# Performance work log

Measured on AMD Instinct MI355X. Metric: run time of the kernel, lower is better.

The kernel has to match this reference:

```python
import jax, jax.numpy as jnp
import numpy as np

N, M, D = 2048, 100000, 128
K = 5


def setup_inputs() -> dict:
    key = jax.random.key(0)
    k1, k2 = jax.random.split(key)
    features = jax.random.normal(k1, (N, D), dtype=jnp.float32)
    memory_bank = jax.random.normal(k2, (M, D), dtype=jnp.float32)
    # normalization buffers computed during fit(); use plausible scalars
    min_val = jnp.zeros((), dtype=jnp.float32)
    max_val = jnp.ones((), dtype=jnp.float32)
    return {
        "features": features,
        "memory_bank": memory_bank,
        "min_val": min_val,
        "max_val": max_val,
        "n_neighbors": K,
    }


def reference(features, memory_bank, min_val, max_val, n_neighbors):
    x2 = jnp.sum(features * features, axis=1, keepdims=True)        # (N,1)
    y2 = jnp.sum(memory_bank * memory_bank, axis=1)[None, :]        # (1,M)
    d2 = x2 + y2 - 2.0 * (features @ memory_bank.T)                 # (N,M)
    dist = jnp.sqrt(jnp.maximum(d2, 0.0))
    # k smallest distances per query (topk largest=False)
    neg_knn, _ = jax.lax.top_k(-dist, n_neighbors)                  # (N,K)
    knn = -neg_knn
    # min-max normalization with fitted stats
    knn = (knn - min_val) / (max_val - min_val)
    return knn.mean(axis=1)                                         # (N,)
```

## Files before the change

### kernel.cpp

```cpp
#include <hip/hip_runtime.h>
#include <stdint.h>

#define N_Q 2048
#define M_B 100000
#define D_DIM 128
#define KNN 5
#define SLABS_TOTAL 1563
#define M_PAD (SLABS_TOTAL * 64)
#define CHUNKS 56
#define SPC 28
#define PPC 14
#define FTOT (CHUNKS * PPC)
#define ROWBLOCKS 16
#define TROWS 128
#define BIGF 3.0e38f
#define NEGF -3.0e38f


typedef __attribute__((ext_vector_type(8))) short short8;
typedef __attribute__((ext_vector_type(4))) unsigned short ushort4v;
typedef __attribute__((ext_vector_type(8))) unsigned short ushort8v;
typedef __attribute__((ext_vector_type(4))) float f32x4;

static __device__ __forceinline__ unsigned short f2bf(float f) {
  unsigned int u = __builtin_bit_cast(unsigned int, f);
  u = (u + 0x7FFFu + ((u >> 16) & 1u)) >> 16;
  return (unsigned short)u;
}

static __device__ __forceinline__ void gload_lds16(const void* g, void* l) {
  __builtin_amdgcn_global_load_lds((const __attribute__((address_space(1))) unsigned int*)g,
                                   (__attribute__((address_space(3))) unsigned int*)l, 16, 0, 0);
}
static __device__ __forceinline__ void gload_lds4(const void* g, void* l) {
  __builtin_amdgcn_global_load_lds((const __attribute__((address_space(1))) unsigned int*)g,
                                   (__attribute__((address_space(3))) unsigned int*)l, 4, 0, 0);
}

#define DPPMAX(v, ctrl)                                                              \
  do {                                                                               \
    int _t = __builtin_amdgcn_update_dpp(0, __builtin_bit_cast(int, (v)), (ctrl),    \
                                         0xf, 0xf, false);                           \
    (v) = fmaxf((v), __builtin_bit_cast(float, _t));                                 \
  } while (0)
#define DPPADD(v, ctrl)                                                              \
  do {                                                                               \
    int _t = __builtin_amdgcn_update_dpp(0, __builtin_bit_cast(int, (v)), (ctrl),    \
                                         0xf, 0xf, false);                           \
    (v) = (v) + __builtin_bit_cast(float, _t);                                       \
  } while (0)

__global__ __launch_bounds__(256) void k_prep(const float* __restrict__ Y,
                                              unsigned short* __restrict__ ybf,
                                              float* __restrict__ ny2) {
  const int s = blockIdx.x;
  const int t = threadIdx.x;
  __shared__ __align__(16) unsigned short tile[8192];
  __shared__ float redy[64 * 33];
#pragma unroll
  for (int i = 0; i < 8; ++i) {
    const int u = i * 256 + t;
    const int rowl = u >> 5;
    const int q = u & 31;
    const int rowg = s * 64 + rowl;
    const int rowc = (rowg < M_B) ? rowg : (M_B - 1);
    const float4 v = ((const float4*)Y)[(size_t)rowc * 32 + q];
    redy[rowl * 33 + q] = v.x * v.x + v.y * v.y + v.z * v.z + v.w * v.w;
    ushort4v o;
    o[0] = f2bf(v.x); o[1] = f2bf(v.y); o[2] = f2bf(v.z); o[3] = f2bf(v.w);
    *(ushort4v*)(tile + (size_t)(((q >> 1) * 64 + rowl) * 8 + (q & 1) * 4)) = o;
  }
  __syncthreads();
  {
    const int rowl = t >> 2;
    const int k = t & 3;
    float ss = 0.f;
#pragma unroll
    for (int j = 0; j < 8; ++j) ss += redy[rowl * 33 + k * 8 + j];
    DPPADD(ss, 0xB1);
    DPPADD(ss, 0x4E);
    const int rowg = s * 64 + rowl;
    if ((t & 3) == 0) ny2[(size_t)s * 64 + rowl] = (rowg < M_B) ? (-0.5f * ss) : NEGF;
  }
#pragma unroll
  for (int i = 0; i < 4; ++i) {
    const int u = i * 256 + t;
    *(ushort8v*)(ybf + ((size_t)s * 1024 + u) * 8) = *(const ushort8v*)(tile + u * 8);
  }
}

__global__ __launch_bounds__(256, 4) void k_main(const float* __restrict__ X,
                                                 const unsigned short* __restrict__ ybf,
                                                 const float* __restrict__ ny2,
                                                 float* __restrict__ rsm) {
  __shared__ __align__(16) char smem[33280];
  unsigned short* ys = (unsigned short*)smem;
  float* ny2s = (float*)(smem + 32768);

  const int bid = blockIdx.x;
  const int chunk = bid % CHUNKS;
  const int rowblock = bid / CHUNKS;
  const int row0 = rowblock * TROWS;

  const int cs0 = chunk * SPC;
  int nslab = SLABS_TOTAL - cs0;
  if (nslab > SPC) nslab = SPC;

  const int t = threadIdx.x;
  const int wave = t >> 6;
  const int lane = t & 63;
  const int lm = lane & 15;
  const int lq = lane >> 4;

  float nx2r[2][4];
  {
    float* red = (float*)smem;
    const int r = t >> 1, h = t & 1;
    const float4* xp = (const float4*)(X + (size_t)(row0 + r) * D_DIM + h * 64);
    float ss = 0.f;
#pragma unroll
    for (int i = 0; i < 16; ++i) {
      const float4 v = xp[i];
      ss += v.x * v.x + v.y * v.y + v.z * v.z + v.w * v.w;
    }
    red[t] = ss;
    __syncthreads();
#pragma unroll
    for (int rt = 0; rt < 2; ++rt)
#pragma unroll
      for (int rr = 0; rr < 4; ++rr) {
        const int rl = wave * 32 + rt * 16 + lq * 4 + rr;
        nx2r[rt][rr] = -0.5f * (red[rl * 2] + red[rl * 2 + 1]);
      }
    __syncthreads();
  }

  short8 afrag[2][4];
#pragma unroll
  for (int rt = 0; rt < 2; ++rt)
#pragma unroll
    for (int ks = 0; ks < 4; ++ks) {
      const float* xr = X + (size_t)(row0 + wave * 32 + rt * 16 + lm) * D_DIM + ks * 32 + lq * 8;
      const float4 a = *(const float4*)xr;
      const float4 b = *(const float4*)(xr + 4);
      short8 f;
      f[0] = (short)f2bf(a.x); f[1] = (short)f2bf(a.y);
      f[2] = (short)f2bf(a.z); f[3] = (short)f2bf(a.w);
      f[4] = (short)f2bf(b.x); f[5] = (short)f2bf(b.y);
      f[6] = (short)f2bf(b.z); f[7] = (short)f2bf(b.w);
      afrag[rt][ks] = f;
    }

  float pmax_r[8];
#pragma unroll
  for (int i = 0; i < 8; ++i) pmax_r[i] = NEGF;

  for (int s = 0; s < nslab; s += 2) {
    const int sg0 = cs0 + s;
    const int two = (s + 1 < nslab);
#pragma unroll
    for (int sl = 0; sl < 2; ++sl) {
      if (sl && !two) break;
      const unsigned short* src = ybf + (size_t)(sg0 + sl) * 8192;
#pragma unroll
      for (int i = 0; i < 4; ++i) {
        const int ub = i * 256 + wave * 64;
        gload_lds16(src + (size_t)(ub + lane) * 8, ys + (size_t)(sl * 8192 + ub * 8));
      }
    }
    if (wave == 0) {
      gload_lds4(ny2 + (size_t)sg0 * 64 + lane, ny2s);
      if (two) gload_lds4(ny2 + (size_t)(sg0 + 1) * 64 + lane, ny2s + 64);
    }
    __syncthreads();

    float prmax[2][4];
#pragma unroll
    for (int rt = 0; rt < 2; ++rt)
#pragma unroll
      for (int rr = 0; rr < 4; ++rr) prmax[rt][rr] = NEGF;

#pragma unroll
    for (int sl = 0; sl < 2; ++sl) {
      if (sl && !two) break;
      float y2c[4];
#pragma unroll
      for (int ct = 0; ct < 4; ++ct) y2c[ct] = ny2s[sl * 64 + ct * 16 + lm];

      f32x4 acc[2][4];
#pragma unroll
      for (int rt = 0; rt < 2; ++rt)
#pragma unroll
        for (int ct = 0; ct < 4; ++ct)
#pragma unroll
          for (int rr = 0; rr < 4; ++rr) acc[rt][ct][rr] = nx2r[rt][rr] + y2c[ct];

#pragma unroll
      for (int ct = 0; ct < 4; ++ct) {
        short8 bfr[4];
#pragma unroll
        for (int ks = 0; ks < 4; ++ks)
          bfr[ks] = *(const short8*)(ys + (size_t)(sl * 8192 +
                       (((ks * 4 + lq) * 64 + ct * 16 + lm)) * 8));
#pragma unroll
        for (int rt = 0; rt < 2; ++rt)
#pragma unroll
          for (int ks = 0; ks < 4; ++ks)
            acc[rt][ct] = __builtin_amdgcn_mfma_f32_16x16x32_bf16(afrag[rt][ks], bfr[ks],
                                                                  acc[rt][ct], 0, 0, 0);
      }

#pragma unroll
      for (int rt = 0; rt < 2; ++rt)
#pragma unroll
        for (int rr = 0; rr < 4; ++rr) {
          const float cm = fmaxf(fmaxf(fmaxf(acc[rt][0][rr], acc[rt][1][rr]),
                                       acc[rt][2][rr]), acc[rt][3][rr]);
          prmax[rt][rr] = fmaxf(prmax[rt][rr], cm);
        }
    }

    const int pl = s >> 1;
#pragma unroll
    for (int rt = 0; rt < 2; ++rt)
#pragma unroll
      for (int rr = 0; rr < 4; ++rr) {
        float v = prmax[rt][rr];
        DPPMAX(v, 0xB1);
        DPPMAX(v, 0x4E);
        DPPMAX(v, 0x141);
        DPPMAX(v, 0x140);
        if (lm == pl) pmax_r[rt * 4 + rr] = v;
      }
    __syncthreads();
  }

  if (lm < PPC) {
#pragma unroll
    for (int rt = 0; rt < 2; ++rt)
#pragma unroll
      for (int rr = 0; rr < 4; ++rr) {
        const int lrow = wave * 32 + rt * 16 + lq * 4 + rr;
        rsm[(size_t)(row0 + lrow) * FTOT + chunk * PPC + lm] = pmax_r[rt * 4 + rr];
      }
  }
}

__global__ __launch_bounds__(256) void k_scan(const float* __restrict__ rsm,
                                              const float* __restrict__ minp,
                                              const float* __restrict__ maxp,
                                              float* __restrict__ out) {
  const int wave = threadIdx.x >> 6;
  const int lane = threadIdx.x & 63;
  const int row = blockIdx.x * 4 + wave;
  const float* rp = rsm + (size_t)row * FTOT;

  float t0 = NEGF, t1 = NEGF, t2 = NEGF, t3 = NEGF, t4 = NEGF;
  for (int i = lane; i < FTOT; i += 64) {
    const float v = rp[i];
    if (v > t4) {
      float m = v;
      float n3 = fminf(t3, m); m = fmaxf(t3, m);
      float n2 = fminf(t2, m); m = fmaxf(t2, m);
      float n1 = fminf(t1, m); m = fmaxf(t1, m);
      float n0 = fminf(t0, m); m = fmaxf(t0, m);
      t0 = m; t1 = n0; t2 = n1; t3 = n2; t4 = n3;
    }
  }

  int k = 0;
  float sum = 0.f;
#pragma unroll
  for (int r = 0; r < KNN; ++r) {
    float head = (k == 0) ? t0 : (k == 1) ? t1 : (k == 2) ? t2 : (k == 3) ? t3
               : (k == 4) ? t4 : NEGF;
    float m = head;
#pragma unroll
    for (int off = 1; off < 64; off <<= 1) m = fmaxf(m, __shfl_xor(m, off));
    const unsigned long long mask = __ballot(head == m);
    const int first = __ffsll(mask) - 1;
    if (lane == first) ++k;
    sum += sqrtf(fmaxf(-2.f * m, 0.f));
  }
  if (lane == 0) {
    const float mn = minp[0], mx = maxp[0];
    out[row] = (sum * (1.0f / KNN) - mn) / (mx - mn);
  }
}

extern "C" void kernel_launch(void* const* d_in, const int* in_sizes, int n_in,
                              void* d_out, int out_size, void* d_ws, size_t ws_size,
                              hipStream_t stream) {
  const float* X = (const float*)d_in[0];
  const float* Y = (const float*)d_in[1];
  const float* minp = (const float*)d_in[2];
  const float* maxp = (const float*)d_in[3];
  float* out = (float*)d_out;

  char* ws = (char*)d_ws;
  size_t off = 0;
  unsigned short* ybf = (unsigned short*)(ws + off); off += (size_t)M_PAD * D_DIM * 2;
  float* ny2 = (float*)(ws + off);                   off += (size_t)M_PAD * 4;
  float* rsm = (float*)(ws + off);                   off += (size_t)N_Q * FTOT * 4;

  k_prep<<<dim3(SLABS_TOTAL), dim3(256), 0, stream>>>(Y, ybf, ny2);
  k_main<<<dim3(ROWBLOCKS * CHUNKS), dim3(256), 0, stream>>>(X, ybf, ny2, rsm);
  k_scan<<<dim3(N_Q / 4), dim3(256), 0, stream>>>(rsm, minp, maxp, out);
}
```

Measured before the change: 166.0 us.

## Defer query norm to scan kernel and rebalance chunk partitioning

Removes the per-block computation of query squared norms (and its two barriers) from the main GEMM kernel. The row-constant |x|^2 term cannot change the top-k order, so it is added back once per row in the scan kernel. Chunk count also goes from 56 to 64, with fewer slabs and partials per chunk, which gives more blocks and better balance across CUs. The risk is a small precision difference, since the row constant is now added after the max search instead of inside the accumulator.

```diff
diff --git a/kernel.cpp b/kernel.cpp
--- a/kernel.cpp
+++ b/kernel.cpp
@@ -7,9 +7,9 @@
 #define KNN 5
 #define SLABS_TOTAL 1563
 #define M_PAD (SLABS_TOTAL * 64)
-#define CHUNKS 56
-#define SPC 28
-#define PPC 14
+#define CHUNKS 64
+#define SPC 25
+#define PPC 13
 #define FTOT (CHUNKS * PPC)
 #define ROWBLOCKS 16
 #define TROWS 128
@@ -112,29 +112,6 @@
   const int lm = lane & 15;
   const int lq = lane >> 4;
 
-  float nx2r[2][4];
-  {
-    float* red = (float*)smem;
-    const int r = t >> 1, h = t & 1;
-    const float4* xp = (const float4*)(X + (size_t)(row0 + r) * D_DIM + h * 64);
-    float ss = 0.f;
-#pragma unroll
-    for (int i = 0; i < 16; ++i) {
-      const float4 v = xp[i];
-      ss += v.x * v.x + v.y * v.y + v.z * v.z + v.w * v.w;
-    }
-    red[t] = ss;
-    __syncthreads();
-#pragma unroll
-    for (int rt = 0; rt < 2; ++rt)
-#pragma unroll
-      for (int rr = 0; rr < 4; ++rr) {
-        const int rl = wave * 32 + rt * 16 + lq * 4 + rr;
-        nx2r[rt][rr] = -0.5f * (red[rl * 2] + red[rl * 2 + 1]);
-      }
-    __syncthreads();
-  }
-
   short8 afrag[2][4];
 #pragma unroll
   for (int rt = 0; rt < 2; ++rt)
@@ -193,7 +170,7 @@
 #pragma unroll
         for (int ct = 0; ct < 4; ++ct)
 #pragma unroll
-          for (int rr = 0; rr < 4; ++rr) acc[rt][ct][rr] = nx2r[rt][rr] + y2c[ct];
+          for (int rr = 0; rr < 4; ++rr) acc[rt][ct][rr] = y2c[ct];
 
 #pragma unroll
       for (int ct = 0; ct < 4; ++ct) {
@@ -247,6 +224,7 @@
 }
 
 __global__ __launch_bounds__(256) void k_scan(const float* __restrict__ rsm,
+                                              const float* __restrict__ X,
                                               const float* __restrict__ minp,
                                               const float* __restrict__ maxp,
                                               float* __restrict__ out) {
@@ -254,6 +232,15 @@
   const int lane = threadIdx.x & 63;
   const int row = blockIdx.x * 4 + wave;
   const float* rp = rsm + (size_t)row * FTOT;
+
+  float x2;
+  {
+    const float a = X[(size_t)row * D_DIM + lane];
+    const float b = X[(size_t)row * D_DIM + 64 + lane];
+    x2 = a * a + b * b;
+#pragma unroll
+    for (int off = 1; off < 64; off <<= 1) x2 += __shfl_xor(x2, off);
+  }
 
   float t0 = NEGF, t1 = NEGF, t2 = NEGF, t3 = NEGF, t4 = NEGF;
   for (int i = lane; i < FTOT; i += 64) {
@@ -280,7 +267,7 @@
     const unsigned long long mask = __ballot(head == m);
     const int first = __ffsll(mask) - 1;
     if (lane == first) ++k;
-    sum += sqrtf(fmaxf(-2.f * m, 0.f));
+    sum += sqrtf(fmaxf(x2 - 2.f * m, 0.f));
   }
   if (lane == 0) {
     const float mn = minp[0], mx = maxp[0];
@@ -305,5 +292,5 @@
 
   k_prep<<<dim3(SLABS_TOTAL), dim3(256), 0, stream>>>(Y, ybf, ny2);
   k_main<<<dim3(ROWBLOCKS * CHUNKS), dim3(256), 0, stream>>>(X, ybf, ny2, rsm);
-  k_scan<<<dim3(N_Q / 4), dim3(256), 0, stream>>>(rsm, minp, maxp, out);
-}
+  k_scan<<<dim3(N_Q / 4), dim3(256), 0, stream>>>(rsm, X, minp, maxp, out);
+}
```

New measurement: 154.6 us. -6.8%, faster.
